# Kernel tuning notes

Hardware: AMD Instinct MI355X
Metric: run time of the kernel (lower is better)

The kernel has to match this reference:

```python
import jax, jax.numpy as jnp
import numpy as np

DIM = 16      # must equal K*K per the module's reshape structure
K = 4         # kernel_size
HEADS = 8
SCALE = (DIM // HEADS) ** (-0.5)


def setup_inputs() -> dict:
    key = jax.random.key(0)
    k1, k2 = jax.random.split(key)
    x = jax.random.normal(k1, (2, 64, 67, 67), dtype=jnp.float32)
    # torch Linear(dim, 3*dim, bias=False) weight: [3*dim, dim]
    w_qkv = jax.random.normal(k2, (3 * DIM, DIM), dtype=jnp.float32) * 0.1
    return {"x": x, "w_qkv": w_qkv}


def reference(x, w_qkv):
    B, C, H, W = x.shape
    k = K
    Ho, Wo = H - k + 1, W - k + 1          # unfold output grid (stride=1)
    L = Ho * Wo
    # Unfold: patches[b, c, i*k+j, ph, pw] = x[b, c, ph+i, pw+j]
    # (matches torch F.unfold channel ordering c-major, then i, then j)
    patches = jnp.stack(
        [x[:, :, i:i + Ho, j:j + Wo] for i in range(k) for j in range(k)],
        axis=2,
    )  # [B, C, k*k, Ho, Wo]
    seq = L // (k * k)                      # L must be divisible by k*k
    # [B*C*k*k, seq, k*k] -- flatten (Ho,Wo)->L row-major then split into (seq, k*k)
    xu = patches.reshape(B * C * k * k, seq, k * k)
    # tiny attention over each row; feature dim = k*k = DIM
    qkv = xu @ w_qkv.T                      # [N, seq, 3*DIM]
    q, kk_, v = jnp.split(qkv, 3, axis=-1)
    scores = jnp.einsum('nqd,nkd->nqk', q, kk_) * SCALE   # [N, seq, seq]
    attn = jax.nn.softmax(scores, axis=-1)                # dropout = identity (eval)
    ao = jnp.einsum('nqk,nkd->nqd', attn, v)              # [N, seq, DIM]
    ao = ao.reshape(B, C, k, k, Ho, Wo)
    # overlap-add fold back onto the HxW grid
    out = jnp.zeros_like(x)
    for i in range(k):
        for j in range(k):
            out = out.at[:, :, i:Ho + i, j:Wo + j].add(ao[:, :, i, j])
    return out
```

## Files before the change

### kernel.cpp

```cpp
#include <hip/hip_runtime.h>


#define BATCH 2
#define CHAN 64
#define HWDIM 67
#define DIM 16
#define PLANE 4096
#define OUT_TOTAL (BATCH * CHAN * HWDIM * HWDIM)
#define ATT_SCALE 0.70710678118654752f
#define LOG2E 1.44269504088896340736f

typedef _Float16 half4 __attribute__((ext_vector_type(4)));
typedef _Float16 half8 __attribute__((ext_vector_type(8)));
typedef float float4v __attribute__((ext_vector_type(4)));
typedef __fp16 fp16x2 __attribute__((ext_vector_type(2)));
typedef unsigned int uint2v __attribute__((ext_vector_type(2)));

static __device__ __forceinline__ half4 mk_half4(float a, float b, float c, float d) {
    fp16x2 lo = __builtin_amdgcn_cvt_pkrtz(a, b);
    fp16x2 hi = __builtin_amdgcn_cvt_pkrtz(c, d);
    uint2v u;
    u[0] = __builtin_bit_cast(unsigned int, lo);
    u[1] = __builtin_bit_cast(unsigned int, hi);
    return __builtin_bit_cast(half4, u);
}

static __device__ __forceinline__ half4 pack4(float4v c) {
    return mk_half4(c[0], c[1], c[2], c[3]);
}

static __device__ __forceinline__ void att_step(const half4 vf, const float4v sfr,
                                                float& l, float4v& oacc) {
    const float p0 = __builtin_amdgcn_exp2f(sfr[0]);
    const float p1 = __builtin_amdgcn_exp2f(sfr[1]);
    const float p2 = __builtin_amdgcn_exp2f(sfr[2]);
    const float p3 = __builtin_amdgcn_exp2f(sfr[3]);
    l += (p0 + p1) + (p2 + p3);
    const half4 pb = mk_half4(p0, p1, p2, p3);
    oacc = __builtin_amdgcn_mfma_f32_16x16x16f16(vf, pb, oacc, 0, 0, 0);
}

__global__ __launch_bounds__(256, 4) void ska_attn(
    const float* __restrict__ x,
    const float* __restrict__ w,
    _Float16* __restrict__ ao)
{
    __shared__ __align__(16) _Float16 qlds[4][16][64][4];

    const int b  = (int)(blockIdx.x & 7) * 64 + (int)(blockIdx.x >> 3);
    const int bc = b >> 2;
    const int ii = b & 3;

    const int tid  = threadIdx.x;
    const int wave = tid >> 6;
    const int lane = tid & 63;
    const int o = lane & 15;
    const int g = lane >> 4;
    const int jj = wave;

    const float4 wq4 = *(const float4*)(w + ( 0 + o) * DIM + 4 * g);
    const float4 wk4 = *(const float4*)(w + (16 + o) * DIM + 4 * g);
    const float4 wv4 = *(const float4*)(w + (32 + o) * DIM + 4 * g);
    const half4 wqf = mk_half4(wq4.x * (ATT_SCALE * LOG2E), wq4.y * (ATT_SCALE * LOG2E),
                               wq4.z * (ATT_SCALE * LOG2E), wq4.w * (ATT_SCALE * LOG2E));
    const half4 wkf = mk_half4(wk4.x, wk4.y, wk4.z, wk4.w);
    const half4 wvf = mk_half4(wv4.x, wv4.y, wv4.z, wv4.w);

    const float4v zf = (float4v){0.f, 0.f, 0.f, 0.f};

    const float* xb = x + ((size_t)bc * HWDIM + ii) * HWDIM + (o & 3) * 16 + 4 * g + jj;
    half4 kf[16], vf[16];
#pragma unroll
    for (int t = 0; t < 16; ++t) {
        const float* xp = xb + (4 * t + (o >> 2)) * HWDIM;
        const half4 xf = mk_half4(xp[0], xp[1], xp[2], xp[3]);
        kf[t] = pack4(__builtin_amdgcn_mfma_f32_16x16x16f16(wkf, xf, zf, 0, 0, 0));
        vf[t] = pack4(__builtin_amdgcn_mfma_f32_16x16x16f16(xf, wvf, zf, 0, 0, 0));
        const half4 qf = pack4(__builtin_amdgcn_mfma_f32_16x16x16f16(wqf, xf, zf, 0, 0, 0));
        *(half4*)&qlds[wave][t][lane][0] = qf;
    }

    const int n = bc * 16 + ii * 4 + jj;
    _Float16* aop = ao + (size_t)n * PLANE;

    for (int jq = 0; jq < 16; jq += 2) {
        const half4 qp0 = *(const half4*)&qlds[wave][jq][lane][0];
        const half4 qp1 = *(const half4*)&qlds[wave][jq + 1][lane][0];
        float4v oacc0 = zf, oacc1 = zf;
        float l0 = 0.f, l1 = 0.f;
#pragma unroll
        for (int t = 0; t < 16; ++t) {
            const float4v s0 = __builtin_amdgcn_mfma_f32_16x16x16f16(kf[t], qp0, zf, 0, 0, 0);
            const float4v s1 = __builtin_amdgcn_mfma_f32_16x16x16f16(kf[t], qp1, zf, 0, 0, 0);
            att_step(vf[t], s0, l0, oacc0);
            att_step(vf[t], s1, l1, oacc1);
        }
#pragma unroll
        for (int u = 0; u < 2; ++u) {
            float lj = u ? l1 : l0;
            lj += __shfl_xor(lj, 16, 64);
            lj += __shfl_xor(lj, 32, 64);
            const float rl = __builtin_amdgcn_rcpf(lj);
            const float4v oa = u ? oacc1 : oacc0;
            const int query = (jq + u) * 16 + o;
            *(half4*)(aop + query * DIM + 4 * g) =
                mk_half4(oa[0] * rl, oa[1] * rl, oa[2] * rl, oa[3] * rl);
        }
    }
}

__global__ __launch_bounds__(256) void ska_sum(
    const _Float16* __restrict__ ao,
    float* __restrict__ out)
{
    const int idx = (int)(blockIdx.x * 256 + threadIdx.x);
    if (idx >= OUT_TOTAL) return;
    const int bc  = idx / (HWDIM * HWDIM);
    const int rem = idx % (HWDIM * HWDIM);
    const int h   = rem / HWDIM;
    const int ww  = rem % HWDIM;
    float acc = 0.f;
#pragma unroll
    for (int i = 0; i < 4; ++i) {
        const int hp = h - i;
        if (hp < 0 || hp >= 64) continue;
#pragma unroll
        for (int j = 0; j < 4; ++j) {
            const int wp = ww - j;
            if (wp < 0 || wp >= 64) continue;
            const int n = bc * 16 + i * 4 + j;
            const int q = (hp << 2) + (wp >> 4);
            const int d = wp & 15;
            acc += (float)ao[(size_t)n * PLANE + q * DIM + d];
        }
    }
    out[idx] = acc;
}

__global__ __launch_bounds__(512, 4) void ska_fused_atomic(
    const float* __restrict__ x, const float* __restrict__ w,
    float* __restrict__ out)
{
    __shared__ __align__(16) _Float16 buf[2][16][64][8];
    __shared__ float fold[64][69];

    const int b  = (int)(blockIdx.x & 7) * 64 + (int)(blockIdx.x >> 3);
    const int bc = b >> 2;
    const int ii = b & 3;
    const int tid  = threadIdx.x;
    const int wave = tid >> 6;
    const int lane = tid & 63;
    const int o = lane & 15;
    const int g = lane >> 4;

    {
        float* ff = &fold[0][0];
        for (int i = tid; i < 64 * 69; i += 512) ff[i] = 0.f;
    }

    const float4 wq4 = *(const float4*)(w + ( 0 + o) * DIM + 4 * g);
    const float4 wk4 = *(const float4*)(w + (16 + o) * DIM + 4 * g);
    const float4 wv4 = *(const float4*)(w + (32 + o) * DIM + 4 * g);
    const half4 wqf = mk_half4(wq4.x * (ATT_SCALE * LOG2E), wq4.y * (ATT_SCALE * LOG2E),
                               wq4.z * (ATT_SCALE * LOG2E), wq4.w * (ATT_SCALE * LOG2E));
    const half4 wkf = mk_half4(wk4.x, wk4.y, wk4.z, wk4.w);
    const half4 wvf = mk_half4(wv4.x, wv4.y, wv4.z, wv4.w);
    const float4v zf = (float4v){0.f, 0.f, 0.f, 0.f};

    const float* xb = x + ((size_t)bc * HWDIM + ii) * HWDIM + (o & 3) * 16 + 4 * g;
    const int roff0 = (8 * wave + (o >> 2)) * HWDIM;
    const int roff1 = roff0 + 4 * HWDIM;

    float xr0a = xb[roff0 + 0], xr0b = xb[roff0 + 1],
          xr0c = xb[roff0 + 2], xr0d = xb[roff0 + 3];
    float xr1a = xb[roff1 + 0], xr1b = xb[roff1 + 1],
          xr1c = xb[roff1 + 2], xr1d = xb[roff1 + 3];

    for (int jj = 0; jj < 4; ++jj) {
        const int cur = jj & 1;
        half4 qfr0, qfr1;
        {
            const half4 xf0 = mk_half4(xr0a, xr0b, xr0c, xr0d);
            const half4 kf0 = pack4(__builtin_amdgcn_mfma_f32_16x16x16f16(wkf, xf0, zf, 0, 0, 0));
            const half4 vf0 = pack4(__builtin_amdgcn_mfma_f32_16x16x16f16(xf0, wvf, zf, 0, 0, 0));
            *(half8*)&buf[cur][2 * wave][lane][0] =
                __builtin_shufflevector(kf0, vf0, 0, 1, 2, 3, 4, 5, 6, 7);
            qfr0 = pack4(__builtin_amdgcn_mfma_f32_16x16x16f16(wqf, xf0, zf, 0, 0, 0));
            const half4 xf1 = mk_half4(xr1a, xr1b, xr1c, xr1d);
            const half4 kf1 = pack4(__builtin_amdgcn_mfma_f32_16x16x16f16(wkf, xf1, zf, 0, 0, 0));
            const half4 vf1 = pack4(__builtin_amdgcn_mfma_f32_16x16x16f16(xf1, wvf, zf, 0, 0, 0));
            *(half8*)&buf[cur][2 * wave + 1][lane][0] =
                __builtin_shufflevector(kf1, vf1, 0, 1, 2, 3, 4, 5, 6, 7);
            qfr1 = pack4(__builtin_amdgcn_mfma_f32_16x16x16f16(wqf, xf1, zf, 0, 0, 0));
        }
        if (jj < 3) {
            const int d = jj + 1;
            xr0a = xb[roff0 + d + 0]; xr0b = xb[roff0 + d + 1];
            xr0c = xb[roff0 + d + 2]; xr0d = xb[roff0 + d + 3];
            xr1a = xb[roff1 + d + 0]; xr1b = xb[roff1 + d + 1];
            xr1c = xb[roff1 + d + 2]; xr1d = xb[roff1 + d + 3];
        }
        __syncthreads();

        float4v oacc0 = zf, oacc1 = zf;
        float l0 = 0.f, l1 = 0.f;
        half8 kvc = *(const half8*)&buf[cur][0][lane][0];
#pragma unroll 4
        for (int t = 0; t < 16; ++t) {
            const half8 kvn = *(const half8*)&buf[cur][(t + 1) & 15][lane][0];
            const half4 kf = __builtin_shufflevector(kvc, kvc, 0, 1, 2, 3);
            const half4 vf = __builtin_shufflevector(kvc, kvc, 4, 5, 6, 7);
            const float4v s0 = __builtin_amdgcn_mfma_f32_16x16x16f16(kf, qfr0, zf, 0, 0, 0);
            const float4v s1 = __builtin_amdgcn_mfma_f32_16x16x16f16(kf, qfr1, zf, 0, 0, 0);
            att_step(vf, s0, l0, oacc0);
            att_step(vf, s1, l1, oacc1);
            kvc = kvn;
        }
#pragma unroll
        for (int u = 0; u < 2; ++u) {
            float lj = u ? l1 : l0;
            lj += __shfl_xor(lj, 16, 64);
            lj += __shfl_xor(lj, 32, 64);
            const float rl = __builtin_amdgcn_rcpf(lj);
            const float4v oa = u ? oacc1 : oacc0;
            const int r = 8 * wave + 4 * u + (o >> 2);
            const int c = 16 * (o & 3) + 4 * g + jj;
            fold[r][c + 0] += oa[0] * rl;
            fold[r][c + 1] += oa[1] * rl;
            fold[r][c + 2] += oa[2] * rl;
            fold[r][c + 3] += oa[3] * rl;
        }
    }
    __syncthreads();

    float* ob = out + ((size_t)bc * HWDIM + ii) * HWDIM;
    for (int i = tid; i < 64 * HWDIM; i += 512) {
        atomicAdd(&ob[i], fold[i / HWDIM][i % HWDIM]);
    }
}

extern "C" void kernel_launch(void* const* d_in, const int* in_sizes, int n_in,
                              void* d_out, int out_size, void* d_ws, size_t ws_size,
                              hipStream_t stream) {
    const float* x = (const float*)d_in[0];
    const float* w = (const float*)d_in[1];
    float* out = (float*)d_out;
    (void)in_sizes; (void)n_in;

    const size_t need = (size_t)BATCH * CHAN * 16 * PLANE * sizeof(_Float16);
    if (ws_size >= need) {
        _Float16* ao = (_Float16*)d_ws;
        ska_attn<<<BATCH * CHAN * 4, 256, 0, stream>>>(x, w, ao);
        ska_sum<<<(OUT_TOTAL + 255) / 256, 256, 0, stream>>>(ao, out);
    } else {
        (void)hipMemsetAsync(out, 0, (size_t)out_size * sizeof(float), stream);
        ska_fused_atomic<<<BATCH * CHAN * 4, 512, 0, stream>>>(x, w, out);
    }
}
```

Baseline: 95.55 us.

## Split queries across twice as many blocks and compute softmax row sums via MFMA

The attention kernel now launches twice as many blocks, and each wave handles half of the 16 query tiles for one (ii, jj) sequence. Each wave still computes the full K/V fragments, so that projection work is duplicated across the two halves. The softmax denominator is now accumulated with an extra MFMA against a ones vector, which replaces the scalar adds and the cross-lane shuffle reduction. The aim is more parallelism and shorter per-wave serial loops, paid for with redundant K/V projection, extra x reads and one more MFMA per step.

```diff
diff --git a/kernel.cpp b/kernel.cpp
--- a/kernel.cpp
+++ b/kernel.cpp
@@ -29,15 +29,16 @@
     return mk_half4(c[0], c[1], c[2], c[3]);
 }
 
-static __device__ __forceinline__ void att_step(const half4 vf, const float4v sfr,
-                                                float& l, float4v& oacc) {
+static __device__ __forceinline__ void att_step2(const half4 vf, const half4 ones,
+                                                 const float4v sfr,
+                                                 float4v& lacc, float4v& oacc) {
     const float p0 = __builtin_amdgcn_exp2f(sfr[0]);
     const float p1 = __builtin_amdgcn_exp2f(sfr[1]);
     const float p2 = __builtin_amdgcn_exp2f(sfr[2]);
     const float p3 = __builtin_amdgcn_exp2f(sfr[3]);
-    l += (p0 + p1) + (p2 + p3);
     const half4 pb = mk_half4(p0, p1, p2, p3);
     oacc = __builtin_amdgcn_mfma_f32_16x16x16f16(vf, pb, oacc, 0, 0, 0);
+    lacc = __builtin_amdgcn_mfma_f32_16x16x16f16(ones, pb, lacc, 0, 0, 0);
 }
 
 __global__ __launch_bounds__(256, 4) void ska_attn(
@@ -45,18 +46,21 @@
     const float* __restrict__ w,
     _Float16* __restrict__ ao)
 {
-    __shared__ __align__(16) _Float16 qlds[4][16][64][4];
-
-    const int b  = (int)(blockIdx.x & 7) * 64 + (int)(blockIdx.x >> 3);
-    const int bc = b >> 2;
-    const int ii = b & 3;
+    __shared__ __align__(16) _Float16 qlds[4][8][64][4];
+
+    const int b  = (int)(blockIdx.x & 7) * 128 + (int)(blockIdx.x >> 3);
+    const int bc = b >> 3;
+    const int ii = (b >> 1) & 3;
+    const int bh = b & 1;
 
     const int tid  = threadIdx.x;
     const int wave = tid >> 6;
     const int lane = tid & 63;
     const int o = lane & 15;
     const int g = lane >> 4;
-    const int jj = wave;
+    const int task = bh * 4 + wave;
+    const int jj = task >> 1;
+    const int qh = task & 1;
 
     const float4 wq4 = *(const float4*)(w + ( 0 + o) * DIM + 4 * g);
     const float4 wk4 = *(const float4*)(w + (16 + o) * DIM + 4 * g);
@@ -76,33 +80,38 @@
         const half4 xf = mk_half4(xp[0], xp[1], xp[2], xp[3]);
         kf[t] = pack4(__builtin_amdgcn_mfma_f32_16x16x16f16(wkf, xf, zf, 0, 0, 0));
         vf[t] = pack4(__builtin_amdgcn_mfma_f32_16x16x16f16(xf, wvf, zf, 0, 0, 0));
+    }
+#pragma unroll
+    for (int u = 0; u < 8; ++u) {
+        const int t = 8 * qh + u;
+        const float* xp = xb + (4 * t + (o >> 2)) * HWDIM;
+        const half4 xf = mk_half4(xp[0], xp[1], xp[2], xp[3]);
         const half4 qf = pack4(__builtin_amdgcn_mfma_f32_16x16x16f16(wqf, xf, zf, 0, 0, 0));
-        *(half4*)&qlds[wave][t][lane][0] = qf;
+        *(half4*)&qlds[wave][u][lane][0] = qf;
     }
 
     const int n = bc * 16 + ii * 4 + jj;
     _Float16* aop = ao + (size_t)n * PLANE;
-
-    for (int jq = 0; jq < 16; jq += 2) {
-        const half4 qp0 = *(const half4*)&qlds[wave][jq][lane][0];
-        const half4 qp1 = *(const half4*)&qlds[wave][jq + 1][lane][0];
-        float4v oacc0 = zf, oacc1 = zf;
-        float l0 = 0.f, l1 = 0.f;
+    const half4 ones = {(_Float16)1.f, (_Float16)1.f, (_Float16)1.f, (_Float16)1.f};
+
+#pragma unroll
+    for (int jp = 0; jp < 4; ++jp) {
+        const half4 qp0 = *(const half4*)&qlds[wave][2 * jp][lane][0];
+        const half4 qp1 = *(const half4*)&qlds[wave][2 * jp + 1][lane][0];
+        float4v oacc0 = zf, oacc1 = zf, lacc0 = zf, lacc1 = zf;
 #pragma unroll
         for (int t = 0; t < 16; ++t) {
             const float4v s0 = __builtin_amdgcn_mfma_f32_16x16x16f16(kf[t], qp0, zf, 0, 0, 0);
             const float4v s1 = __builtin_amdgcn_mfma_f32_16x16x16f16(kf[t], qp1, zf, 0, 0, 0);
-            att_step(vf[t], s0, l0, oacc0);
-            att_step(vf[t], s1, l1, oacc1);
+            att_step2(vf[t], ones, s0, lacc0, oacc0);
+            att_step2(vf[t], ones, s1, lacc1, oacc1);
         }
 #pragma unroll
         for (int u = 0; u < 2; ++u) {
-            float lj = u ? l1 : l0;
-            lj += __shfl_xor(lj, 16, 64);
-            lj += __shfl_xor(lj, 32, 64);
+            const float4v oa = u ? oacc1 : oacc0;
+            const float lj  = u ? lacc1[0] : lacc0[0];
             const float rl = __builtin_amdgcn_rcpf(lj);
-            const float4v oa = u ? oacc1 : oacc0;
-            const int query = (jq + u) * 16 + o;
+            const int query = (8 * qh + 2 * jp + u) * 16 + o;
             *(half4*)(aop + query * DIM + 4 * g) =
                 mk_half4(oa[0] * rl, oa[1] * rl, oa[2] * rl, oa[3] * rl);
         }
@@ -212,8 +221,20 @@
             const half4 vf = __builtin_shufflevector(kvc, kvc, 4, 5, 6, 7);
             const float4v s0 = __builtin_amdgcn_mfma_f32_16x16x16f16(kf, qfr0, zf, 0, 0, 0);
             const float4v s1 = __builtin_amdgcn_mfma_f32_16x16x16f16(kf, qfr1, zf, 0, 0, 0);
-            att_step(vf, s0, l0, oacc0);
-            att_step(vf, s1, l1, oacc1);
+            const float p00 = __builtin_amdgcn_exp2f(s0[0]);
+            const float p01 = __builtin_amdgcn_exp2f(s0[1]);
+            const float p02 = __builtin_amdgcn_exp2f(s0[2]);
+            const float p03 = __builtin_amdgcn_exp2f(s0[3]);
+            l0 += (p00 + p01) + (p02 + p03);
+            oacc0 = __builtin_amdgcn_mfma_f32_16x16x16f16(
+                vf, mk_half4(p00, p01, p02, p03), oacc0, 0, 0, 0);
+            const float p10 = __builtin_amdgcn_exp2f(s1[0]);
+            const float p11 = __builtin_amdgcn_exp2f(s1[1]);
+            const float p12 = __builtin_amdgcn_exp2f(s1[2]);
+            const float p13 = __builtin_amdgcn_exp2f(s1[3]);
+            l1 += (p10 + p11) + (p12 + p13);
+            oacc1 = __builtin_amdgcn_mfma_f32_16x16x16f16(
+                vf, mk_half4(p10, p11, p12, p13), oacc1, 0, 0, 0);
             kvc = kvn;
         }
 #pragma unroll
@@ -250,7 +271,7 @@
     const size_t need = (size_t)BATCH * CHAN * 16 * PLANE * sizeof(_Float16);
     if (ws_size >= need) {
         _Float16* ao = (_Float16*)d_ws;
-        ska_attn<<<BATCH * CHAN * 4, 256, 0, stream>>>(x, w, ao);
+        ska_attn<<<BATCH * CHAN * 8, 256, 0, stream>>>(x, w, ao);
         ska_sum<<<(OUT_TOTAL + 255) / 256, 256, 0, stream>>>(ao, out);
     } else {
         (void)hipMemsetAsync(out, 0, (size_t)out_size * sizeof(float), stream);
```

After: 95.51 us. Within noise of the previous version (-0.0%).
